# Kernel optimization log

Hardware: AMD Instinct MI355X
Metric: run time of the kernel (lower is better)

The kernel has to match this reference:

```python
import jax, jax.numpy as jnp
import numpy as np

MAX_DEG = 10  # deepchem GraphConv default max_deg
EPS = 1e-5


def _neighbor_sum(h, adj, deg):
    # h: [B,N,F], adj: [B,N,K] padded neighbor indices, deg: [B,N]
    B = h.shape[0]
    g = h[jnp.arange(B)[:, None, None], adj]  # [B,N,K,F] irregular gather
    mask = (jnp.arange(MAX_DEG)[None, None, :] < deg[:, :, None]).astype(h.dtype)
    return jnp.einsum('bnkf,bnk->bnf', g, mask)


def _graph_conv(h, adj, deg, W_neigh, W_self, b_neigh, b_self):
    # Degree-bucketed conv: atoms of degree d use W_self[d] (and W_neigh[d-1] if d>=1)
    ns = _neighbor_sum(h, adj, deg)  # [B,N,F]
    out = jnp.zeros(h.shape[:-1] + (W_self.shape[-1],), h.dtype)
    for d in range(MAX_DEG + 1):
        m = (deg == d)[..., None].astype(h.dtype)
        t = h @ W_self[d] + b_self[d]
        if d >= 1:
            t = t + ns @ W_neigh[d - 1] + b_neigh[d - 1]
        out = out + m * t
    return out


def _batch_norm(h, gamma, beta):
    # training-mode batch norm over (batch, atom) for each feature channel
    mu = jnp.mean(h, axis=(0, 1), keepdims=True)
    var = jnp.var(h, axis=(0, 1), keepdims=True)
    return (h - mu) * jax.lax.rsqrt(var + EPS) * gamma + beta


def setup_inputs() -> dict:
    key = jax.random.key(0)
    ks = jax.random.split(key, 12)
    B, N, F, H, T = 128, 512, 75, 128, 12
    x = jax.random.normal(ks[0], (B, N, F), dtype=jnp.float32)
    adjacency_list = jax.random.randint(ks[1], (B, N, MAX_DEG), 0, N)
    degree_list = jax.random.randint(ks[2], (B, N), 0, MAX_DEG + 1)
    s1 = 1.0 / np.sqrt(F)
    s2 = 1.0 / np.sqrt(H)
    return {
        'x': x,
        'adjacency_list': adjacency_list,
        'degree_list': degree_list,
        'W_neigh1': jax.random.normal(ks[3], (MAX_DEG, F, H), dtype=jnp.float32) * s1,
        'W_self1': jax.random.normal(ks[4], (MAX_DEG + 1, F, H), dtype=jnp.float32) * s1,
        'b_neigh1': jnp.zeros((MAX_DEG, H), jnp.float32),
        'b_self1': jnp.zeros((MAX_DEG + 1, H), jnp.float32),
        'gamma1': jnp.ones((H,), jnp.float32),
        'beta1': jnp.zeros((H,), jnp.float32),
        'W_neigh2': jax.random.normal(ks[5], (MAX_DEG, H, H), dtype=jnp.float32) * s2,
        'W_self2': jax.random.normal(ks[6], (MAX_DEG + 1, H, H), dtype=jnp.float32) * s2,
        'b_neigh2': jnp.zeros((MAX_DEG, H), jnp.float32),
        'b_self2': jnp.zeros((MAX_DEG + 1, H), jnp.float32),
        'gamma2': jnp.ones((H,), jnp.float32),
        'beta2': jnp.zeros((H,), jnp.float32),
        'W_dense': jax.random.normal(ks[7], (H, T), dtype=jnp.float32) * s2,
        'b_dense': jnp.zeros((T,), jnp.float32),
    }


def reference(x, adjacency_list, degree_list,
              W_neigh1, W_self1, b_neigh1, b_self1, gamma1, beta1,
              W_neigh2, W_self2, b_neigh2, b_self2, gamma2, beta2,
              W_dense, b_dense):
    h = _graph_conv(x, adjacency_list, degree_list, W_neigh1, W_self1, b_neigh1, b_self1)
    h = jax.nn.relu(_batch_norm(h, gamma1, beta1))
    h = _graph_conv(h, adjacency_list, degree_list, W_neigh2, W_self2, b_neigh2, b_self2)
    h = jax.nn.relu(_batch_norm(h, gamma2, beta2))
    # dropout is identity at inference
    h = jnp.mean(h, axis=1)  # graph-level mean pool over atoms -> [B,H]
    return h @ W_dense + b_dense  # [B, n_tasks]
```

## Files before the change

kernel.cpp:

```cpp
#include <hip/hip_runtime.h>

#define NODES   65536
#define NGRAPH  512
#define BATCH   128
#define HID     128
#define TOUT    12
#define MAXDEG  10
#define NDEG    11
#define EPSV    1e-5f
#define MT      64
#define NTILES  (NODES / MT + NDEG)
#define PCAP    1056

typedef float f32x4 __attribute__((ext_vector_type(4)));

__device__ __forceinline__ f32x4 ntload(const float* p) {
    return __builtin_nontemporal_load((const f32x4*)p);
}
__device__ __forceinline__ void ntstore(float* p, f32x4 v) {
    __builtin_nontemporal_store(v, (f32x4*)p);
}

__global__ void k_zero(f32x4* part4, float* stats1, float* stats2, int* cnt) {
    int i = blockIdx.x * 256 + threadIdx.x;
    part4[i] = 0.f;
    if (blockIdx.x == 0) {
        stats1[threadIdx.x] = 0.f;
        stats2[threadIdx.x] = 0.f;
        if (threadIdx.x < 16) cnt[threadIdx.x] = 0;
    }
}

__global__ void k_bucket(const int* __restrict__ deg, int* __restrict__ cnt,
                         int* __restrict__ lists) {
    __shared__ int s_cnt[NDEG];
    __shared__ int s_base[NDEG];
    int t = threadIdx.x;
    if (t < NDEG) s_cnt[t] = 0;
    __syncthreads();
    int i = blockIdx.x * 256 + t;
    int d = deg[i];
    d = d < 0 ? 0 : (d > MAXDEG ? MAXDEG : d);
    int pos = atomicAdd(&s_cnt[d], 1);
    __syncthreads();
    if (t < NDEG) s_base[t] = atomicAdd(&cnt[t], s_cnt[t]);
    __syncthreads();
    lists[d * NODES + s_base[d] + pos] = i;
}

__global__ void k_plan(const int* __restrict__ cnt, int* __restrict__ offs) {
    if (threadIdx.x == 0) {
        int acc = 0;
        offs[0] = 0;
        for (int d = 0; d < NDEG; ++d) {
            acc += (cnt[d] + MT - 1) / MT;
            offs[d + 1] = acc;
        }
    }
}

__global__ void k_build1(const float* __restrict__ Ws, const float* __restrict__ Wn,
                         float* __restrict__ Wcat) {
    int idx = blockIdx.x * 256 + threadIdx.x;
    int h4 = idx & 31;
    int k  = (idx >> 5) % 160;
    int d  = idx / (160 * 32);
    f32x4 v = 0.f;
    if (k < 75)
        v = *(const f32x4*)(Ws + ((size_t)d * 75 + k) * 128 + h4 * 4);
    else if (k >= 80 && k < 155 && d >= 1)
        v = *(const f32x4*)(Wn + ((size_t)(d - 1) * 75 + (k - 80)) * 128 + h4 * 4);
    *(f32x4*)(Wcat + ((size_t)d * 160 + k) * 128 + h4 * 4) = v;
}
__global__ void k_build2(const float* __restrict__ Ws, const float* __restrict__ Wn,
                         float* __restrict__ Wcat) {
    int idx = blockIdx.x * 256 + threadIdx.x;
    int h4 = idx & 31;
    int k  = (idx >> 5) & 255;
    int d  = idx >> 13;
    f32x4 v = 0.f;
    if (k < 128)
        v = *(const f32x4*)(Ws + ((size_t)d * 128 + k) * 128 + h4 * 4);
    else if (d >= 1)
        v = *(const f32x4*)(Wn + ((size_t)(d - 1) * 128 + (k - 128)) * 128 + h4 * 4);
    *(f32x4*)(Wcat + ((size_t)d * 256 + k) * 128 + h4 * 4) = v;
}
__global__ void k_bias(const float* bs1, const float* bn1, const float* bs2, const float* bn2,
                       float* bcat1, float* bcat2) {
    int d = blockIdx.x, t = threadIdx.x;
    if (t < 128) bcat1[d * 128 + t] = bs1[d * 128 + t] + (d > 0 ? bn1[(d - 1) * 128 + t] : 0.f);
    else { int h = t - 128; bcat2[d * 128 + h] = bs2[d * 128 + h] + (d > 0 ? bn2[(d - 1) * 128 + h] : 0.f); }
}

__global__ void k_ns1(const float* __restrict__ x, const int* __restrict__ adj,
                      const int* __restrict__ deg, float* __restrict__ feats1) {
    int idx = blockIdx.x * 256 + threadIdx.x;
    int node = idx / 20;
    int q = idx - node * 20;
    int f = q * 4;
    int d = deg[node];
    d = d < 0 ? 0 : (d > MAXDEG ? MAXDEG : d);
    const int* arow = adj + node * MAXDEG;
    int base = node & ~(NGRAPH - 1);
    f32x4 s = 0.f;
    for (int k = 0; k < d; ++k) {
        const float* xr = x + (size_t)(base + arow[k]) * 75 + f;
        if (f + 3 < 75) { s.x += xr[0]; s.y += xr[1]; s.z += xr[2]; s.w += xr[3]; }
        else {
            if (f + 0 < 75) s.x += xr[0];
            if (f + 1 < 75) s.y += xr[1];
            if (f + 2 < 75) s.z += xr[2];
        }
    }
    *(f32x4*)(feats1 + (size_t)node * 160 + 80 + f) = s;
    f32x4 v = 0.f;
    const float* xs = x + (size_t)node * 75 + f;
    if (f + 3 < 75) { v.x = xs[0]; v.y = xs[1]; v.z = xs[2]; v.w = xs[3]; }
    else {
        if (f + 0 < 75) v.x = xs[0];
        if (f + 1 < 75) v.y = xs[1];
        if (f + 2 < 75) v.z = xs[2];
    }
    *(f32x4*)(feats1 + (size_t)node * 160 + f) = v;
}

__global__ void k_ns2(const float* __restrict__ feats2r, const int* __restrict__ adj,
                      const int* __restrict__ deg, float* __restrict__ feats2w) {
    int idx = blockIdx.x * 256 + threadIdx.x;
    int node = idx >> 5;
    int f = (idx & 31) * 4;
    int d = deg[node];
    d = d < 0 ? 0 : (d > MAXDEG ? MAXDEG : d);
    const int* arow = adj + node * MAXDEG;
    int base = node & ~(NGRAPH - 1);
    f32x4 s = 0.f;
    for (int k = 0; k < d; ++k) {
        f32x4 v = *(const f32x4*)(feats2r + (size_t)(base + arow[k]) * 256 + f);
        s += v;
    }
    *(f32x4*)(feats2w + (size_t)node * 256 + 128 + f) = s;
}

template<int S, int OS>
__global__ __launch_bounds__(256, 6)
void k_conv(const float* __restrict__ feats, const float* __restrict__ Wcat,
            const float* __restrict__ bcat, const int* __restrict__ lists,
            const int* __restrict__ cnt, const int* __restrict__ offs,
            float* __restrict__ out, float* __restrict__ partials) {
    constexpr int NCH = S / 16;

    __shared__ int   s_ids[MT];
    __shared__ float sW[2][16][128];
    __shared__ float sF[2][16][68];

    const int bid = blockIdx.x;
    if (bid >= offs[NDEG]) return;
    int d = 0;
    #pragma unroll
    for (int q = 1; q < NDEG; ++q) d += (bid >= offs[q]);
    const int c  = cnt[d];
    const int m0 = (bid - offs[d]) * MT;
    const int mv = min(MT, c - m0);
    const int t  = threadIdx.x;

    if (t < MT) s_ids[t] = lists[d * NODES + m0 + (t < mv ? t : 0)];
    __syncthreads();

    const int kw = t >> 5;
    const int c4 = t & 31;
    const int frow = t >> 2;
    const int kq = t & 3;
    const float* Wbase = Wcat + (size_t)d * S * 128;
    const float* Frow = feats + (size_t)s_ids[frow] * S;

    f32x4 w0, w1, f0;
    auto LOAD = [&](int ch) {
        const float* wp = Wbase + (size_t)(ch * 16 + kw) * 128 + c4 * 4;
        w0 = *(const f32x4*)(wp);
        w1 = *(const f32x4*)(wp + 8 * 128);
        f0 = ntload(Frow + ch * 16 + kq * 4);
    };
    auto STORE = [&](int buf) {
        *(f32x4*)&sW[buf][kw][c4 * 4]     = w0;
        *(f32x4*)&sW[buf][kw + 8][c4 * 4] = w1;
        sF[buf][kq * 4 + 0][frow] = f0.x;
        sF[buf][kq * 4 + 1][frow] = f0.y;
        sF[buf][kq * 4 + 2][frow] = f0.z;
        sF[buf][kq * 4 + 3][frow] = f0.w;
    };

    const int cg = t & 31;
    const int rg = t >> 5;

    f32x4 acc[8];
    {
        f32x4 b = *(const f32x4*)(bcat + d * HID + cg * 4);
        #pragma unroll
        for (int j = 0; j < 8; ++j) acc[j] = b;
    }

    LOAD(0); STORE(0);
    __syncthreads();

    for (int ch = 0; ch < NCH; ++ch) {
        const int buf = ch & 1;
        const bool more = (ch + 1 < NCH);
        if (more) LOAD(ch + 1);
        #pragma unroll 8
        for (int k = 0; k < 16; ++k) {
            f32x4 wv = *(const f32x4*)&sW[buf][k][cg * 4];
            f32x4 fA = *(const f32x4*)&sF[buf][k][rg * 8];
            f32x4 fB = *(const f32x4*)&sF[buf][k][rg * 8 + 4];
            acc[0] += fA.x * wv;
            acc[1] += fA.y * wv;
            acc[2] += fA.z * wv;
            acc[3] += fA.w * wv;
            acc[4] += fB.x * wv;
            acc[5] += fB.y * wv;
            acc[6] += fB.z * wv;
            acc[7] += fB.w * wv;
        }
        if (more) STORE(buf ^ 1);
        __syncthreads();
    }

    f32x4 cs = 0.f, cq = 0.f;
    #pragma unroll
    for (int j = 0; j < 8; ++j) {
        int i = rg * 8 + j;
        if (i < mv) {
            ntstore(out + (size_t)s_ids[i] * OS + cg * 4, acc[j]);
            cs += acc[j];
            cq += acc[j] * acc[j];
        }
    }
    __syncthreads();
    float* red = &sW[0][0][0];
    *(f32x4*)&red[rg * 256 + cg * 4]       = cs;
    *(f32x4*)&red[rg * 256 + 128 + cg * 4] = cq;
    __syncthreads();
    {
        float tot = 0.f;
        #pragma unroll
        for (int g = 0; g < 8; ++g) tot += red[g * 256 + t];
        partials[(size_t)bid * 256 + t] = tot;
    }
}

__global__ void k_redstats(float* __restrict__ partials, float* __restrict__ stats) {
    int t = threadIdx.x;
    float acc = 0.f;
    for (int bx = blockIdx.x; bx < PCAP; bx += gridDim.x) {
        float* p = partials + (size_t)bx * 256 + t;
        acc += *p;
        *p = 0.f;
    }
    atomicAdd(&stats[t], acc);
}

__global__ void k_bnrelu(float* __restrict__ feats2, const float* __restrict__ stats,
                         const float* __restrict__ gamma, const float* __restrict__ beta) {
    int idx = blockIdx.x * 256 + threadIdx.x;
    int node = idx >> 5;
    int c4 = (idx & 31) * 4;
    float* p = feats2 + (size_t)node * 256 + c4;
    f32x4 v = *(f32x4*)p;
    const float inv = 1.f / (float)NODES;
    #pragma unroll
    for (int j = 0; j < 4; ++j) {
        int col = c4 + j;
        float mu  = stats[col] * inv;
        float var = stats[HID + col] * inv - mu * mu;
        float rs  = rsqrtf(var + EPSV);
        float sc  = gamma[col] * rs;
        float sh  = beta[col] - mu * sc;
        v[j] = fmaxf(fmaf(v[j], sc, sh), 0.f);
    }
    *(f32x4*)p = v;
}

__global__ void k_pool_dense(const float* __restrict__ h2, const float* __restrict__ stats,
                             const float* __restrict__ gamma, const float* __restrict__ beta,
                             const float* __restrict__ Wd, const float* __restrict__ bd,
                             float* __restrict__ outp) {
    __shared__ float s_part[4][HID];
    __shared__ float s_pool[HID];
    const int b = blockIdx.x;
    const int t = threadIdx.x;
    const int hcol = t & (HID - 1);
    const int q = t >> 7;
    const float inv = 1.f / (float)NODES;
    float mu  = stats[hcol] * inv;
    float var = stats[HID + hcol] * inv - mu * mu;
    float rs  = rsqrtf(var + EPSV);
    float sc  = gamma[hcol] * rs;
    float sh  = beta[hcol] - mu * sc;
    float acc = 0.f;
    const float* hp = h2 + ((size_t)b * NGRAPH + q * 128) * HID + hcol;
    #pragma unroll 4
    for (int n = 0; n < 128; ++n)
        acc += fmaxf(fmaf(hp[(size_t)n * HID], sc, sh), 0.f);
    s_part[q][hcol] = acc;
    __syncthreads();
    if (t < HID)
        s_pool[t] = (s_part[0][t] + s_part[1][t] + s_part[2][t] + s_part[3][t]) * (1.f / NGRAPH);
    __syncthreads();
    if (t < TOUT) {
        float o = bd[t];
        for (int hh = 0; hh < HID; ++hh)
            o = fmaf(s_pool[hh], Wd[hh * TOUT + t], o);
        outp[b * TOUT + t] = o;
    }
}

extern "C" void kernel_launch(void* const* d_in, const int* in_sizes, int n_in,
                              void* d_out, int out_size, void* d_ws, size_t ws_size,
                              hipStream_t stream) {
    const float* x   = (const float*)d_in[0];
    const int*   adj = (const int*)d_in[1];
    const int*   deg = (const int*)d_in[2];
    const float* Wn1 = (const float*)d_in[3];
    const float* Ws1 = (const float*)d_in[4];
    const float* bn1 = (const float*)d_in[5];
    const float* bs1 = (const float*)d_in[6];
    const float* g1  = (const float*)d_in[7];
    const float* be1 = (const float*)d_in[8];
    const float* Wn2 = (const float*)d_in[9];
    const float* Ws2 = (const float*)d_in[10];
    const float* bn2 = (const float*)d_in[11];
    const float* bs2 = (const float*)d_in[12];
    const float* g2  = (const float*)d_in[13];
    const float* be2 = (const float*)d_in[14];
    const float* Wd  = (const float*)d_in[15];
    const float* bd  = (const float*)d_in[16];

    float* ws     = (float*)d_ws;
    float* feats1 = ws;
    float* h2     = ws;
    float* feats2 = ws + 10485760;
    float* Wcat1  = ws + 27262976;
    float* Wcat2  = ws + 27488256;
    float* bcat1  = ws + 27848704;
    float* bcat2  = ws + 27850112;
    float* part   = ws + 27851520;
    float* stats1 = ws + 28121856;
    float* stats2 = ws + 28122112;
    int*   cnt    = (int*)(ws + 28122368);
    int*   offs   = cnt + 16;
    int*   lists  = cnt + 32;

    k_zero<<<PCAP / 4, 256, 0, stream>>>((f32x4*)part, stats1, stats2, cnt);
    k_bucket<<<NODES / 256, 256, 0, stream>>>(deg, cnt, lists);
    k_plan<<<1, 64, 0, stream>>>(cnt, offs);
    k_build1<<<220, 256, 0, stream>>>(Ws1, Wn1, Wcat1);
    k_build2<<<352, 256, 0, stream>>>(Ws2, Wn2, Wcat2);
    k_bias<<<NDEG, 256, 0, stream>>>(bs1, bn1, bs2, bn2, bcat1, bcat2);

    k_ns1<<<NODES * 20 / 256, 256, 0, stream>>>(x, adj, deg, feats1);
    k_conv<160, 256><<<NTILES, 256, 0, stream>>>(feats1, Wcat1, bcat1,
                                                 lists, cnt, offs, feats2, part);
    k_redstats<<<32, 256, 0, stream>>>(part, stats1);
    k_bnrelu<<<8192, 256, 0, stream>>>(feats2, stats1, g1, be1);

    k_ns2<<<8192, 256, 0, stream>>>(feats2, adj, deg, feats2);
    k_conv<256, 128><<<NTILES, 256, 0, stream>>>(feats2, Wcat2, bcat2,
                                                 lists, cnt, offs, h2, part);
    k_redstats<<<32, 256, 0, stream>>>(part, stats2);

    k_pool_dense<<<BATCH, 512, 0, stream>>>(h2, stats2, g2, be2, Wd, bd, (float*)d_out);
}
```

Baseline: 352.0 us.

## Fuse BN-ReLU into neighbor-sum and conv loads, enlarge conv tile to 128 rows

Removes the standalone batch-norm+ReLU pass over layer-1 output. The affine scale and shift are precomputed once by a tiny kernel and applied on the fly when the neighbor-sum and the second conv read h1. Layer-1 output and the neighbor sums now live in separate compact 128-wide buffers instead of one interleaved 256-wide buffer. The conv tile grows from 64 to 128 rows with 8x8 outputs per thread, which improves weight reuse but raises register use (launch bounds lowered to 2) and recomputes BN-ReLU for each gathered neighbor.

```diff
diff --git a/kernel.cpp b/kernel.cpp
--- a/kernel.cpp
+++ b/kernel.cpp
@@ -8,9 +8,9 @@
 #define MAXDEG  10
 #define NDEG    11
 #define EPSV    1e-5f
-#define MT      64
+#define MT      128
 #define NTILES  (NODES / MT + NDEG)
-#define PCAP    1056
+#define PCAP    544
 
 typedef float f32x4 __attribute__((ext_vector_type(4)));
 
@@ -19,6 +19,14 @@
 }
 __device__ __forceinline__ void ntstore(float* p, f32x4 v) {
     __builtin_nontemporal_store(v, (f32x4*)p);
+}
+__device__ __forceinline__ f32x4 bnrelu4(f32x4 v, f32x4 sc, f32x4 sh) {
+    f32x4 r;
+    r.x = fmaxf(fmaf(v.x, sc.x, sh.x), 0.f);
+    r.y = fmaxf(fmaf(v.y, sc.y, sh.y), 0.f);
+    r.z = fmaxf(fmaf(v.z, sc.z, sh.z), 0.f);
+    r.w = fmaxf(fmaf(v.w, sc.w, sh.w), 0.f);
+    return r;
 }
 
 __global__ void k_zero(f32x4* part4, float* stats1, float* stats2, int* cnt) {
@@ -124,8 +132,22 @@
     *(f32x4*)(feats1 + (size_t)node * 160 + f) = v;
 }
 
-__global__ void k_ns2(const float* __restrict__ feats2r, const int* __restrict__ adj,
-                      const int* __restrict__ deg, float* __restrict__ feats2w) {
+__global__ void k_scale(const float* __restrict__ stats, const float* __restrict__ g,
+                        const float* __restrict__ be, float* __restrict__ sc,
+                        float* __restrict__ sh) {
+    int c = threadIdx.x;
+    const float inv = 1.f / (float)NODES;
+    float mu  = stats[c] * inv;
+    float var = stats[HID + c] * inv - mu * mu;
+    float rs  = rsqrtf(var + EPSV);
+    float s   = g[c] * rs;
+    sc[c] = s;
+    sh[c] = be[c] - mu * s;
+}
+
+__global__ void k_ns2(const float* __restrict__ h1, const int* __restrict__ adj,
+                      const int* __restrict__ deg, const float* __restrict__ sc,
+                      const float* __restrict__ sh, float* __restrict__ ns2) {
     int idx = blockIdx.x * 256 + threadIdx.x;
     int node = idx >> 5;
     int f = (idx & 31) * 4;
@@ -133,25 +155,29 @@
     d = d < 0 ? 0 : (d > MAXDEG ? MAXDEG : d);
     const int* arow = adj + node * MAXDEG;
     int base = node & ~(NGRAPH - 1);
+    f32x4 sc4 = *(const f32x4*)(sc + f);
+    f32x4 sh4 = *(const f32x4*)(sh + f);
     f32x4 s = 0.f;
     for (int k = 0; k < d; ++k) {
-        f32x4 v = *(const f32x4*)(feats2r + (size_t)(base + arow[k]) * 256 + f);
-        s += v;
-    }
-    *(f32x4*)(feats2w + (size_t)node * 256 + 128 + f) = s;
-}
-
-template<int S, int OS>
-__global__ __launch_bounds__(256, 6)
-void k_conv(const float* __restrict__ feats, const float* __restrict__ Wcat,
-            const float* __restrict__ bcat, const int* __restrict__ lists,
+        f32x4 v = *(const f32x4*)(h1 + (size_t)(base + arow[k]) * HID + f);
+        s += bnrelu4(v, sc4, sh4);
+    }
+    *(f32x4*)(ns2 + (size_t)node * HID + f) = s;
+}
+
+template<int S, bool BN>
+__global__ __launch_bounds__(256, 2)
+void k_conv(const float* __restrict__ f160, const float* __restrict__ h1,
+            const float* __restrict__ ns2, const float* __restrict__ Wcat,
+            const float* __restrict__ bcat, const float* __restrict__ sc,
+            const float* __restrict__ sh, const int* __restrict__ lists,
             const int* __restrict__ cnt, const int* __restrict__ offs,
             float* __restrict__ out, float* __restrict__ partials) {
     constexpr int NCH = S / 16;
 
     __shared__ int   s_ids[MT];
     __shared__ float sW[2][16][128];
-    __shared__ float sF[2][16][68];
+    __shared__ float sF[2][16][132];
 
     const int bid = blockIdx.x;
     if (bid >= offs[NDEG]) return;
@@ -166,37 +192,60 @@
     if (t < MT) s_ids[t] = lists[d * NODES + m0 + (t < mv ? t : 0)];
     __syncthreads();
 
-    const int kw = t >> 5;
-    const int c4 = t & 31;
-    const int frow = t >> 2;
-    const int kq = t & 3;
+    const int kw = t >> 4;
+    const int cw = (t & 15) * 8;
+    const int fr = t >> 1;
+    const int k8 = (t & 1) * 8;
     const float* Wbase = Wcat + (size_t)d * S * 128;
-    const float* Frow = feats + (size_t)s_ids[frow] * S;
-
-    f32x4 w0, w1, f0;
+    const int fid = s_ids[fr];
+    const float* Frow1 = (S == 160) ? (f160 + (size_t)fid * 160) : nullptr;
+    const float* FrowS = (S == 256) ? (h1 + (size_t)fid * 128) : nullptr;
+    const float* FrowN = (S == 256) ? (ns2 + (size_t)fid * 128) : nullptr;
+
+    f32x4 w0, w1, f0, f1;
     auto LOAD = [&](int ch) {
-        const float* wp = Wbase + (size_t)(ch * 16 + kw) * 128 + c4 * 4;
+        const float* wp = Wbase + (size_t)(ch * 16 + kw) * 128 + cw;
         w0 = *(const f32x4*)(wp);
-        w1 = *(const f32x4*)(wp + 8 * 128);
-        f0 = ntload(Frow + ch * 16 + kq * 4);
+        w1 = *(const f32x4*)(wp + 4);
+        if constexpr (S == 160) {
+            const float* fp = Frow1 + ch * 16 + k8;
+            f0 = ntload(fp);
+            f1 = ntload(fp + 4);
+        } else {
+            if (ch < 8) {
+                const float* fp = FrowS + ch * 16 + k8;
+                f0 = ntload(fp);
+                f1 = ntload(fp + 4);
+                if constexpr (BN) {
+                    int cc = ch * 16 + k8;
+                    f0 = bnrelu4(f0, *(const f32x4*)(sc + cc), *(const f32x4*)(sh + cc));
+                    f1 = bnrelu4(f1, *(const f32x4*)(sc + cc + 4), *(const f32x4*)(sh + cc + 4));
+                }
+            } else {
+                const float* fp = FrowN + (ch - 8) * 16 + k8;
+                f0 = ntload(fp);
+                f1 = ntload(fp + 4);
+            }
+        }
     };
     auto STORE = [&](int buf) {
-        *(f32x4*)&sW[buf][kw][c4 * 4]     = w0;
-        *(f32x4*)&sW[buf][kw + 8][c4 * 4] = w1;
-        sF[buf][kq * 4 + 0][frow] = f0.x;
-        sF[buf][kq * 4 + 1][frow] = f0.y;
-        sF[buf][kq * 4 + 2][frow] = f0.z;
-        sF[buf][kq * 4 + 3][frow] = f0.w;
+        *(f32x4*)&sW[buf][kw][cw]     = w0;
+        *(f32x4*)&sW[buf][kw][cw + 4] = w1;
+        sF[buf][k8 + 0][fr] = f0.x; sF[buf][k8 + 1][fr] = f0.y;
+        sF[buf][k8 + 2][fr] = f0.z; sF[buf][k8 + 3][fr] = f0.w;
+        sF[buf][k8 + 4][fr] = f1.x; sF[buf][k8 + 5][fr] = f1.y;
+        sF[buf][k8 + 6][fr] = f1.z; sF[buf][k8 + 7][fr] = f1.w;
     };
 
-    const int cg = t & 31;
-    const int rg = t >> 5;
-
-    f32x4 acc[8];
+    const int cg = t & 15;
+    const int rg = t >> 4;
+
+    f32x4 acc[8][2];
     {
-        f32x4 b = *(const f32x4*)(bcat + d * HID + cg * 4);
+        f32x4 b0 = *(const f32x4*)(bcat + d * HID + cg * 8);
+        f32x4 b1 = *(const f32x4*)(bcat + d * HID + cg * 8 + 4);
         #pragma unroll
-        for (int j = 0; j < 8; ++j) acc[j] = b;
+        for (int j = 0; j < 8; ++j) { acc[j][0] = b0; acc[j][1] = b1; }
     }
 
     LOAD(0); STORE(0);
@@ -206,43 +255,48 @@
         const int buf = ch & 1;
         const bool more = (ch + 1 < NCH);
         if (more) LOAD(ch + 1);
-        #pragma unroll 8
+        #pragma unroll 4
         for (int k = 0; k < 16; ++k) {
-            f32x4 wv = *(const f32x4*)&sW[buf][k][cg * 4];
+            f32x4 wA = *(const f32x4*)&sW[buf][k][cg * 8];
+            f32x4 wB = *(const f32x4*)&sW[buf][k][cg * 8 + 4];
             f32x4 fA = *(const f32x4*)&sF[buf][k][rg * 8];
             f32x4 fB = *(const f32x4*)&sF[buf][k][rg * 8 + 4];
-            acc[0] += fA.x * wv;
-            acc[1] += fA.y * wv;
-            acc[2] += fA.z * wv;
-            acc[3] += fA.w * wv;
-            acc[4] += fB.x * wv;
-            acc[5] += fB.y * wv;
-            acc[6] += fB.z * wv;
-            acc[7] += fB.w * wv;
+            acc[0][0] += fA.x * wA;  acc[0][1] += fA.x * wB;
+            acc[1][0] += fA.y * wA;  acc[1][1] += fA.y * wB;
+            acc[2][0] += fA.z * wA;  acc[2][1] += fA.z * wB;
+            acc[3][0] += fA.w * wA;  acc[3][1] += fA.w * wB;
+            acc[4][0] += fB.x * wA;  acc[4][1] += fB.x * wB;
+            acc[5][0] += fB.y * wA;  acc[5][1] += fB.y * wB;
+            acc[6][0] += fB.z * wA;  acc[6][1] += fB.z * wB;
+            acc[7][0] += fB.w * wA;  acc[7][1] += fB.w * wB;
         }
         if (more) STORE(buf ^ 1);
         __syncthreads();
     }
 
-    f32x4 cs = 0.f, cq = 0.f;
+    f32x4 cs0 = 0.f, cs1 = 0.f, cq0 = 0.f, cq1 = 0.f;
     #pragma unroll
     for (int j = 0; j < 8; ++j) {
         int i = rg * 8 + j;
         if (i < mv) {
-            ntstore(out + (size_t)s_ids[i] * OS + cg * 4, acc[j]);
-            cs += acc[j];
-            cq += acc[j] * acc[j];
+            float* op = out + (size_t)s_ids[i] * HID + cg * 8;
+            ntstore(op, acc[j][0]);
+            ntstore(op + 4, acc[j][1]);
+            cs0 += acc[j][0]; cs1 += acc[j][1];
+            cq0 += acc[j][0] * acc[j][0]; cq1 += acc[j][1] * acc[j][1];
         }
     }
     __syncthreads();
     float* red = &sW[0][0][0];
-    *(f32x4*)&red[rg * 256 + cg * 4]       = cs;
-    *(f32x4*)&red[rg * 256 + 128 + cg * 4] = cq;
+    *(f32x4*)&red[rg * 256 + cg * 8]           = cs0;
+    *(f32x4*)&red[rg * 256 + cg * 8 + 4]       = cs1;
+    *(f32x4*)&red[rg * 256 + 128 + cg * 8]     = cq0;
+    *(f32x4*)&red[rg * 256 + 128 + cg * 8 + 4] = cq1;
     __syncthreads();
     {
         float tot = 0.f;
         #pragma unroll
-        for (int g = 0; g < 8; ++g) tot += red[g * 256 + t];
+        for (int g = 0; g < 16; ++g) tot += red[g * 256 + t];
         partials[(size_t)bid * 256 + t] = tot;
     }
 }
@@ -256,27 +310,6 @@
         *p = 0.f;
     }
     atomicAdd(&stats[t], acc);
-}
-
-__global__ void k_bnrelu(float* __restrict__ feats2, const float* __restrict__ stats,
-                         const float* __restrict__ gamma, const float* __restrict__ beta) {
-    int idx = blockIdx.x * 256 + threadIdx.x;
-    int node = idx >> 5;
-    int c4 = (idx & 31) * 4;
-    float* p = feats2 + (size_t)node * 256 + c4;
-    f32x4 v = *(f32x4*)p;
-    const float inv = 1.f / (float)NODES;
-    #pragma unroll
-    for (int j = 0; j < 4; ++j) {
-        int col = c4 + j;
-        float mu  = stats[col] * inv;
-        float var = stats[HID + col] * inv - mu * mu;
-        float rs  = rsqrtf(var + EPSV);
-        float sc  = gamma[col] * rs;
-        float sh  = beta[col] - mu * sc;
-        v[j] = fmaxf(fmaf(v[j], sc, sh), 0.f);
-    }
-    *(f32x4*)p = v;
 }
 
 __global__ void k_pool_dense(const float* __restrict__ h2, const float* __restrict__ stats,
@@ -337,15 +370,18 @@
     float* ws     = (float*)d_ws;
     float* feats1 = ws;
     float* h2     = ws;
-    float* feats2 = ws + 10485760;
+    float* h1     = ws + 10485760;
+    float* ns2    = ws + 18874368;
     float* Wcat1  = ws + 27262976;
     float* Wcat2  = ws + 27488256;
     float* bcat1  = ws + 27848704;
     float* bcat2  = ws + 27850112;
     float* part   = ws + 27851520;
-    float* stats1 = ws + 28121856;
-    float* stats2 = ws + 28122112;
-    int*   cnt    = (int*)(ws + 28122368);
+    float* stats1 = ws + 27990784;
+    float* stats2 = ws + 27991040;
+    float* sc1    = ws + 27991296;
+    float* sh1    = ws + 27991424;
+    int*   cnt    = (int*)(ws + 27991552);
     int*   offs   = cnt + 16;
     int*   lists  = cnt + 32;
 
@@ -357,14 +393,16 @@
     k_bias<<<NDEG, 256, 0, stream>>>(bs1, bn1, bs2, bn2, bcat1, bcat2);
 
     k_ns1<<<NODES * 20 / 256, 256, 0, stream>>>(x, adj, deg, feats1);
-    k_conv<160, 256><<<NTILES, 256, 0, stream>>>(feats1, Wcat1, bcat1,
-                                                 lists, cnt, offs, feats2, part);
+    k_conv<160, false><<<NTILES, 256, 0, stream>>>(feats1, nullptr, nullptr, Wcat1, bcat1,
+                                                   nullptr, nullptr, lists, cnt, offs,
+                                                   h1, part);
     k_redstats<<<32, 256, 0, stream>>>(part, stats1);
-    k_bnrelu<<<8192, 256, 0, stream>>>(feats2, stats1, g1, be1);
-
-    k_ns2<<<8192, 256, 0, stream>>>(feats2, adj, deg, feats2);
-    k_conv<256, 128><<<NTILES, 256, 0, stream>>>(feats2, Wcat2, bcat2,
-                                                 lists, cnt, offs, h2, part);
+    k_scale<<<1, 128, 0, stream>>>(stats1, g1, be1, sc1, sh1);
+
+    k_ns2<<<8192, 256, 0, stream>>>(h1, adj, deg, sc1, sh1, ns2);
+    k_conv<256, true><<<NTILES, 256, 0, stream>>>(nullptr, h1, ns2, Wcat2, bcat2,
+                                                  sc1, sh1, lists, cnt, offs,
+                                                  h2, part);
     k_redstats<<<32, 256, 0, stream>>>(part, stats2);
 
     k_pool_dense<<<BATCH, 512, 0, stream>>>(h2, stats2, g2, be2, Wd, bd, (float*)d_out);
```

After: 345.0 us. -2.0%, faster.
